# Kernel tuning notes

Hardware: AMD Instinct MI355X
Metric: run time of the kernel (lower is better)

Reference implementation:

```python
import jax, jax.numpy as jnp
import numpy as np

B, N, C = 1024, 64, 512  # batch, num_classes (graph nodes), in_channels
EPS = 1e-5  # BatchNorm1d default eps


def setup_inputs() -> dict:
    key = jax.random.key(0)
    kx, ku, kv = jax.random.split(key, 3)
    std = float(np.sqrt(2.0 / C))  # matches weight.data.normal_(0, sqrt(2/in_channels))
    return {
        "x": jax.random.normal(kx, (B, N, C), dtype=jnp.float32),
        "U_w": jax.random.normal(ku, (C, C), dtype=jnp.float32) * std,
        "U_b": jnp.zeros((C,), dtype=jnp.float32),
        "V_w": jax.random.normal(kv, (C, C), dtype=jnp.float32) * std,
        "V_b": jnp.zeros((C,), dtype=jnp.float32),
        "bn_w": jnp.ones((N,), dtype=jnp.float32),
        "bn_b": jnp.zeros((N,), dtype=jnp.float32),
        "neighbor_num": 4,
    }


def reference(x, U_w, U_b, V_w, V_b, bn_w, bn_b, neighbor_num):
    # --- dynamic top-k adjacency from dot-product similarity ('dots' metric) ---
    si = jax.lax.stop_gradient(x)                       # x.detach()
    s = jnp.einsum('bic,bjc->bij', si, si)              # [B,N,N] similarity
    thr = jax.lax.top_k(s, neighbor_num)[0][..., -1:]   # k-th largest per row
    adj = (s >= thr).astype(x.dtype)                    # [B,N,N] 0/1 adjacency
    # --- symmetric normalization D^{-1/2} A D^{-1/2} ---
    dinv = jnp.sum(adj, axis=-1) ** -0.5                # [B,N]
    A = adj * dinv[:, :, None] * dinv[:, None, :]       # diag(d) @ A @ diag(d)
    # --- aggregate: A V(x) + U(x) ---
    Vx = x @ V_w.T + V_b                                # [B,N,C]
    agg = jnp.einsum('bij,bjc->bic', A, Vx) + x @ U_w.T + U_b
    # --- BatchNorm1d over channel dim = N (training mode: batch stats over (B,C)) ---
    mean = jnp.mean(agg, axis=(0, 2), keepdims=True)
    var = jnp.mean(jnp.square(agg - mean), axis=(0, 2), keepdims=True)  # biased
    y = (agg - mean) * jax.lax.rsqrt(var + EPS) * bn_w[None, :, None] + bn_b[None, :, None]
    return jax.nn.relu(x + y)
```

## Files before the change

kernel.cpp:

```cpp
#include <hip/hip_runtime.h>
#include <stdint.h>

typedef unsigned short u16;
typedef unsigned int   u32;
typedef unsigned long long u64;

typedef __attribute__((ext_vector_type(8))) short short8;
typedef __attribute__((ext_vector_type(4))) float floatx4;
typedef __attribute__((ext_vector_type(4))) float fx4;
typedef __attribute__((ext_vector_type(2))) double dx2;

#define MFMA16(a,b,c) __builtin_amdgcn_mfma_f32_16x16x32_bf16((a),(b),(c),0,0,0)

#define GLL16(ldsptr, gptr) __builtin_amdgcn_global_load_lds( \
    (const __attribute__((address_space(1))) u32*)(gptr), \
    (__attribute__((address_space(3))) u32*)(ldsptr), 16, 0, 0)

__device__ __forceinline__ u16 f2bf(float f) {
  u32 u = __float_as_uint(f);
  return (u16)((u + 0x7FFFu + ((u >> 16) & 1u)) >> 16);
}
__device__ __forceinline__ short8 mk_frag(u64 lo, u64 hi) {
  union { short8 v; u64 q[2]; } u; u.q[0] = lo; u.q[1] = hi; return u.v;
}
__device__ __forceinline__ u64 pack4bf(float a, float b, float c, float d) {
  return (u64)f2bf(a) | ((u64)f2bf(b) << 16) | ((u64)f2bf(c) << 32) | ((u64)f2bf(d) << 48);
}

__global__ __launch_bounds__(256) void k_wcvt(const float* __restrict__ Uw,
                                              const float* __restrict__ Ub,
                                              const float* __restrict__ Vw,
                                              const float* __restrict__ Vb,
                                              u16* __restrict__ Wvu,
                                              float* __restrict__ biascat,
                                              float* __restrict__ stats) {
  int idx = blockIdx.x * 256 + threadIdx.x;
  int o  = idx >> 7;
  int k4 = (idx & 127) << 2;
  const float* src = (o < 512) ? (Vw + (size_t)o * 512 + k4)
                               : (Uw + (size_t)(o - 512) * 512 + k4);
  fx4 v = *(const fx4*)src;
  *(u64*)(Wvu + (size_t)o * 512 + k4) = pack4bf(v.x, v.y, v.z, v.w);
  if (idx < 1024) {
    biascat[idx] = (idx < 512) ? Vb[idx] : Ub[idx - 512];
    stats[idx] = 0.f;
  }
}

__global__ __launch_bounds__(256) void k_adj(const float* __restrict__ x,
                                             u16* __restrict__ xb16,
                                             u16* __restrict__ A16) {
  const int b = blockIdx.x;
  const int t = threadIdx.x;
  const int ti = t >> 4;
  const int tj = t & 15;

  __shared__ __align__(16) unsigned char smem_adj[33792 + 512 + 512];
  double* xs64     = (double*)smem_adj;
  double* s_lds    = (double*)smem_adj;
  double* thr_lds  = (double*)(smem_adj + 33792);
  double* dinv_lds = (double*)(smem_adj + 33792 + 512);

  const float* xb = x + (size_t)b * 32768;
  u16* xbg = xb16 + (size_t)b * 32768;

  double acc[4][4];
#pragma unroll
  for (int r = 0; r < 4; ++r)
#pragma unroll
    for (int c = 0; c < 4; ++c) acc[r][c] = 0.0;

  for (int k0 = 0; k0 < 512; k0 += 64) {
    __syncthreads();
#pragma unroll
    for (int i = 0; i < 4; ++i) {
      int s  = i * 256 + t;
      int row = s >> 4;
      int q4 = (s & 15) << 2;
      fx4 v = *(const fx4*)(xb + row * 512 + k0 + q4);
      dx2 d0 = {(double)v.x, (double)v.y};
      dx2 d1 = {(double)v.z, (double)v.w};
      *(dx2*)&xs64[row * 66 + q4]     = d0;
      *(dx2*)&xs64[row * 66 + q4 + 2] = d1;
      __builtin_nontemporal_store(pack4bf(v.x, v.y, v.z, v.w),
                                  (u64*)&xbg[row * 512 + k0 + q4]);
    }
    __syncthreads();
#pragma unroll 2
    for (int k = 0; k < 64; k += 4) {
      dx2 av[4][2], bv[4][2];
#pragma unroll
      for (int r = 0; r < 4; ++r) {
        av[r][0] = *(const dx2*)&xs64[(ti * 4 + r) * 66 + k];
        av[r][1] = *(const dx2*)&xs64[(ti * 4 + r) * 66 + k + 2];
      }
#pragma unroll
      for (int c = 0; c < 4; ++c) {
        bv[c][0] = *(const dx2*)&xs64[(tj + 16 * c) * 66 + k];
        bv[c][1] = *(const dx2*)&xs64[(tj + 16 * c) * 66 + k + 2];
      }
#pragma unroll
      for (int r = 0; r < 4; ++r)
#pragma unroll
        for (int c = 0; c < 4; ++c) {
          acc[r][c] += av[r][0][0] * bv[c][0][0];
          acc[r][c] += av[r][0][1] * bv[c][0][1];
          acc[r][c] += av[r][1][0] * bv[c][1][0];
          acc[r][c] += av[r][1][1] * bv[c][1][1];
        }
    }
  }
  __syncthreads();

#pragma unroll
  for (int r = 0; r < 4; ++r)
#pragma unroll
    for (int c = 0; c < 4; ++c)
      s_lds[(ti * 4 + r) * 65 + tj + 16 * c] = acc[r][c];
  __syncthreads();

  if (t < 64) {
    const double* row = &s_lds[t * 65];
    double v0 = -1e300, v1 = -1e300, v2 = -1e300, v3 = -1e300;
    for (int j = 0; j < 64; ++j) {
      double v = row[j];
      if (v > v3) {
        if (v > v2) {
          v3 = v2;
          if (v > v1) { v2 = v1; if (v > v0) { v1 = v0; v0 = v; } else { v1 = v; } }
          else { v2 = v; }
        } else { v3 = v; }
      }
    }
    int d = 0;
    for (int j = 0; j < 64; ++j) d += (row[j] >= v3) ? 1 : 0;
    thr_lds[t] = v3;
    dinv_lds[t] = 1.0 / sqrt((double)d);
  }
  __syncthreads();
  {
    int i = t >> 2;
    int j0 = (t & 3) << 4;
    double thr = thr_lds[i];
    double di = dinv_lds[i];
    const double* row = &s_lds[i * 65];
    u16* dst = A16 + (size_t)b * 4096 + i * 64 + j0;
#pragma unroll
    for (int q = 0; q < 4; ++q) {
      int j = j0 + q * 4;
      float a0 = (row[j + 0] >= thr) ? (float)(di * dinv_lds[j + 0]) : 0.f;
      float a1 = (row[j + 1] >= thr) ? (float)(di * dinv_lds[j + 1]) : 0.f;
      float a2 = (row[j + 2] >= thr) ? (float)(di * dinv_lds[j + 2]) : 0.f;
      float a3 = (row[j + 3] >= thr) ? (float)(di * dinv_lds[j + 3]) : 0.f;
      *(u64*)(dst + q * 4) = pack4bf(a0, a1, a2, a3);
    }
  }
}

__device__ __forceinline__ void stage_tiles(unsigned char* base,
                                            const u16* __restrict__ xrow,
                                            const u16* __restrict__ Wvu,
                                            int c0, int k0,
                                            int w, int lane, int swb) {
#pragma unroll
  for (int i = 0; i < 2; ++i) {
    int chunk = i * 4 + w;
    int r = chunk * 8 + (lane >> 3);
    GLL16(base + chunk * 1024,
          (const unsigned char*)(xrow + r * 512 + k0) + swb);
  }
#pragma unroll
  for (int i = 0; i < 8; ++i) {
    int chunk = i * 4 + w;
    int ol = chunk * 8 + (lane >> 3);
    int o  = (ol < 128) ? (c0 + ol) : (512 + c0 + (ol - 128));
    GLL16(base + 8192 + chunk * 1024,
          (const unsigned char*)(Wvu + (size_t)o * 512 + k0) + swb);
  }
}

__global__ __launch_bounds__(256, 2) void k_gemm(const u16* __restrict__ xb16,
                                                 const u16* __restrict__ Wvu,
                                                 const u16* __restrict__ A16,
                                                 const float* __restrict__ biascat,
                                                 float* __restrict__ stats,
                                                 float* __restrict__ aggout) {
  const int orig = blockIdx.x;
  const int nid  = (orig & 7) * 512 + (orig >> 3);
  const int c0 = (nid & 3) * 128;
  const int b  = nid >> 2;

  const int t = threadIdx.x;
  const int w = t >> 6;
  const int lane = t & 63;
  const int ln = lane & 15;
  const int g4 = (lane >> 4) << 2;
  const int sws = (ln & 7) << 3;
  const int swb = ((lane & 7) ^ (lane >> 3)) << 4;

  __shared__ __align__(16) unsigned char smem[81920];
  u16*   lds_A    = (u16*)smem;
  u16*   lds_p    = (u16*)(smem + 8192);
  float* lds_stat = (float*)(smem + 40448);
  float* lds_out  = (float*)(smem + 40960);

  floatx4 acc[4][4];
#pragma unroll
  for (int mf = 0; mf < 4; ++mf)
#pragma unroll
    for (int nf = 0; nf < 4; ++nf) acc[mf][nf] = (floatx4){0.f, 0.f, 0.f, 0.f};

  const u16* xrow = xb16 + (size_t)b * 32768;

  stage_tiles(smem, xrow, Wvu, c0, 0, w, lane, swb);
  __syncthreads();

  for (int kt = 0; kt < 8; ++kt) {
    unsigned char* cur = smem + ((kt & 1) ? 40960 : 0);
    unsigned char* nxt = smem + ((kt & 1) ? 0 : 40960);

    if (kt < 7) {
      stage_tiles(nxt, xrow, Wvu, c0, (kt + 1) * 64, w, lane, swb);
    } else {
      const unsigned char* srcA = (const unsigned char*)(A16 + (size_t)b * 4096);
#pragma unroll
      for (int i = 0; i < 2; ++i) {
        int chunk = i * 4 + w;
        GLL16(nxt + chunk * 1024,
              srcA + chunk * 1024 + (lane >> 3) * 128 + swb);
      }
    }

    const u16* lds_x = (const u16*)cur;
    const u16* lds_w = (const u16*)(cur + 8192);
#pragma unroll
    for (int kk = 0; kk < 2; ++kk) {
      int kb = kk * 32 + g4;
      int kbs = kb ^ sws;
      short8 af[4];
#pragma unroll
      for (int mf = 0; mf < 4; ++mf) {
        const u16* p = &lds_x[(mf * 16 + ln) * 64];
        af[mf] = mk_frag(*(const u64*)(p + kbs), *(const u64*)(p + (kbs ^ 16)));
      }
#pragma unroll
      for (int nf = 0; nf < 4; ++nf) {
        int ol = (nf < 2) ? (w * 32 + nf * 16 + ln)
                          : (128 + w * 32 + (nf - 2) * 16 + ln);
        const u16* p = &lds_w[ol * 64];
        short8 bf = mk_frag(*(const u64*)(p + kbs), *(const u64*)(p + (kbs ^ 16)));
#pragma unroll
        for (int mf = 0; mf < 4; ++mf)
          acc[mf][nf] = MFMA16(af[mf], bf, acc[mf][nf]);
      }
    }
    __syncthreads();
  }

#pragma unroll
  for (int nf = 0; nf < 4; ++nf) {
    int o = (nf < 2) ? (c0 + w * 32 + nf * 16 + ln)
                     : (512 + c0 + w * 32 + (nf - 2) * 16 + ln);
    float bv = biascat[o];
#pragma unroll
    for (int mf = 0; mf < 4; ++mf)
#pragma unroll
      for (int r = 0; r < 4; ++r) acc[mf][nf][r] += bv;
  }

#pragma unroll
  for (int mf = 0; mf < 4; ++mf)
#pragma unroll
    for (int nf = 0; nf < 2; ++nf) {
      int c  = w * 32 + nf * 16 + ln;
      int j0 = mf * 16 + g4;
      *(u64*)&lds_p[c * 68 + j0] =
          pack4bf(acc[mf][nf][0], acc[mf][nf][1], acc[mf][nf][2], acc[mf][nf][3]);
    }
  if (t < 128) lds_stat[t] = 0.f;
  __syncthreads();

  floatx4 acc2[4][2];
#pragma unroll
  for (int mf = 0; mf < 4; ++mf)
#pragma unroll
    for (int nf = 0; nf < 2; ++nf) acc2[mf][nf] = acc[mf][nf + 2];
#pragma unroll
  for (int kk = 0; kk < 2; ++kk) {
    int kb = kk * 32 + g4;
    int kbs = kb ^ sws;
    short8 af[4];
#pragma unroll
    for (int mf = 0; mf < 4; ++mf) {
      const u16* p = &lds_A[(mf * 16 + ln) * 64];
      af[mf] = mk_frag(*(const u64*)(p + kbs), *(const u64*)(p + (kbs ^ 16)));
    }
#pragma unroll
    for (int nf = 0; nf < 2; ++nf) {
      int c = w * 32 + nf * 16 + ln;
      const u16* p = &lds_p[c * 68 + kb];
      short8 bf = mk_frag(*(const u64*)p, *(const u64*)(p + 16));
#pragma unroll
      for (int mf = 0; mf < 4; ++mf)
        acc2[mf][nf] = MFMA16(af[mf], bf, acc2[mf][nf]);
    }
  }

#pragma unroll
  for (int mf = 0; mf < 4; ++mf) {
#pragma unroll
    for (int r = 0; r < 4; ++r) {
      int i = mf * 16 + g4 + r;
      float v0 = acc2[mf][0][r];
      float v1 = acc2[mf][1][r];
      lds_out[i * 132 + w * 32 + ln]      = v0;
      lds_out[i * 132 + w * 32 + 16 + ln] = v1;
      float s = v0 + v1, ss = v0 * v0 + v1 * v1;
#pragma unroll
      for (int m = 1; m < 16; m <<= 1) { s += __shfl_xor(s, m); ss += __shfl_xor(ss, m); }
      if (ln == 0) {
        atomicAdd(&lds_stat[i * 2 + 0], s);
        atomicAdd(&lds_stat[i * 2 + 1], ss);
      }
    }
  }
  __syncthreads();

  float* outp = aggout + (size_t)b * 32768 + c0;
#pragma unroll
  for (int i8 = 0; i8 < 8; ++i8) {
    int flat = i8 * 256 + t;
    int row = flat >> 5;
    int c4 = (flat & 31) << 2;
    fx4 v = *(const fx4*)&lds_out[row * 132 + c4];
    __builtin_nontemporal_store(v, (fx4*)(outp + (size_t)row * 512 + c4));
  }
  if (t < 64) {
    float* sg = stats + ((size_t)(b & 7) * 64 + t) * 2;
    atomicAdd(&sg[0], lds_stat[t * 2 + 0]);
    atomicAdd(&sg[1], lds_stat[t * 2 + 1]);
  }
}

__global__ void k_bnfin(const float* __restrict__ stats,
                        const float* __restrict__ bnw,
                        const float* __restrict__ bnb,
                        float* __restrict__ params) {
  int t = threadIdx.x;
  if (t >= 64) return;
  float S = 0.f, SS = 0.f;
  for (int g = 0; g < 8; ++g) {
    S  += stats[((size_t)g * 64 + t) * 2 + 0];
    SS += stats[((size_t)g * 64 + t) * 2 + 1];
  }
  const float inv = 1.f / (1024.f * 512.f);
  float mean = S * inv;
  float var = SS * inv - mean * mean;
  float istd = rsqrtf(var + 1e-5f);
  params[t]       = mean;
  params[64 + t]  = istd * bnw[t];
  params[128 + t] = bnb[t];
}

__global__ __launch_bounds__(256) void k_final(const float* __restrict__ x,
                                               const float* __restrict__ params,
                                               float* __restrict__ out) {
  __shared__ float pm[64], psc[64], psh[64];
  if (threadIdx.x < 64) {
    pm[threadIdx.x]  = params[threadIdx.x];
    psc[threadIdx.x] = params[64 + threadIdx.x];
    psh[threadIdx.x] = params[128 + threadIdx.x];
  }
  __syncthreads();
  const size_t total4 = (size_t)1024 * 64 * 512 / 4;
  for (size_t i4 = (size_t)blockIdx.x * 256 + threadIdx.x; i4 < total4;
       i4 += (size_t)gridDim.x * 256) {
    int n = (int)((i4 >> 7) & 63);
    fx4 a  = ((const fx4*)out)[i4];
    fx4 xv = ((const fx4*)x)[i4];
    float m = pm[n], sc = psc[n], sh = psh[n];
    fx4 r;
    r.x = fmaxf(xv.x + (a.x - m) * sc + sh, 0.f);
    r.y = fmaxf(xv.y + (a.y - m) * sc + sh, 0.f);
    r.z = fmaxf(xv.z + (a.z - m) * sc + sh, 0.f);
    r.w = fmaxf(xv.w + (a.w - m) * sc + sh, 0.f);
    ((fx4*)out)[i4] = r;
  }
}

extern "C" void kernel_launch(void* const* d_in, const int* in_sizes, int n_in,
                              void* d_out, int out_size, void* d_ws, size_t ws_size,
                              hipStream_t stream) {
  const float* x   = (const float*)d_in[0];
  const float* Uw  = (const float*)d_in[1];
  const float* Ub  = (const float*)d_in[2];
  const float* Vw  = (const float*)d_in[3];
  const float* Vb  = (const float*)d_in[4];
  const float* bnw = (const float*)d_in[5];
  const float* bnb = (const float*)d_in[6];

  char* ws = (char*)d_ws;
  u16*  xb16    = (u16*)ws;
  u16*  A16     = (u16*)(ws + 67108864);
  u16*  Wvu     = (u16*)(ws + 75497472);
  float* biascat = (float*)(ws + 76546048);
  float* stats   = (float*)(ws + 76550144);
  float* params  = (float*)(ws + 76554240);

  float* agg = (float*)d_out;

  k_wcvt <<<dim3(512),  dim3(256), 0, stream>>>(Uw, Ub, Vw, Vb, Wvu, biascat, stats);
  k_adj  <<<dim3(1024), dim3(256), 0, stream>>>(x, xb16, A16);
  k_gemm <<<dim3(4096), dim3(256), 0, stream>>>(xb16, Wvu, A16, biascat, stats, agg);
  k_bnfin<<<dim3(1),    dim3(64),  0, stream>>>(stats, bnw, bnb, params);
  k_final<<<dim3(2048), dim3(256), 0, stream>>>(x, params, agg);
}
```

Before: 331.5 us.

## Exploit Gram symmetry in adjacency kernel, swizzle LDS, read bf16 x in epilogue

The similarity kernel now computes only the upper-triangular 4x4 tiles of the symmetric Gram matrix with 136 of 256 threads, mirroring results into LDS, and applies an XOR swizzle to the fp64 LDS tile to reduce bank conflicts. The final residual/BN/ReLU kernel reads the bf16 copy of x instead of fp32 x, halving that stream's bytes. The bf16 residual adds rounding error to the output relative to the fp32 reference, and idle threads in the Gram loop reduce parallel utilisation.

```diff
diff --git a/kernel.cpp b/kernel.cpp
--- a/kernel.cpp
+++ b/kernel.cpp
@@ -20,6 +20,7 @@
   u32 u = __float_as_uint(f);
   return (u16)((u + 0x7FFFu + ((u >> 16) & 1u)) >> 16);
 }
+__device__ __forceinline__ float bf2f(u16 h) { return __uint_as_float(((u32)h) << 16); }
 __device__ __forceinline__ short8 mk_frag(u64 lo, u64 hi) {
   union { short8 v; u64 q[2]; } u; u.q[0] = lo; u.q[1] = hi; return u.v;
 }
@@ -52,8 +53,16 @@
                                              u16* __restrict__ A16) {
   const int b = blockIdx.x;
   const int t = threadIdx.x;
-  const int ti = t >> 4;
-  const int tj = t & 15;
+
+  int ti = 0, rem = t, done = 0;
+#pragma unroll
+  for (int r = 0; r < 16; ++r) {
+    int cnt = 16 - r;
+    if (!done) { if (rem < cnt) done = 1; else { rem -= cnt; ti = r + 1; } }
+  }
+  const int tj = ti + rem;
+  const int swa = (ti & 3) << 2;
+  const int swb = (tj & 3) << 2;
 
   __shared__ __align__(16) unsigned char smem_adj[33792 + 512 + 512];
   double* xs64     = (double*)smem_adj;
@@ -77,46 +86,59 @@
       int s  = i * 256 + t;
       int row = s >> 4;
       int q4 = (s & 15) << 2;
+      int qs = q4 ^ (((row >> 2) & 3) << 2);
       fx4 v = *(const fx4*)(xb + row * 512 + k0 + q4);
       dx2 d0 = {(double)v.x, (double)v.y};
       dx2 d1 = {(double)v.z, (double)v.w};
-      *(dx2*)&xs64[row * 66 + q4]     = d0;
-      *(dx2*)&xs64[row * 66 + q4 + 2] = d1;
+      *(dx2*)&xs64[row * 66 + qs]     = d0;
+      *(dx2*)&xs64[row * 66 + qs + 2] = d1;
       __builtin_nontemporal_store(pack4bf(v.x, v.y, v.z, v.w),
                                   (u64*)&xbg[row * 512 + k0 + q4]);
     }
     __syncthreads();
+    if (t < 136) {
 #pragma unroll 2
-    for (int k = 0; k < 64; k += 4) {
-      dx2 av[4][2], bv[4][2];
-#pragma unroll
-      for (int r = 0; r < 4; ++r) {
-        av[r][0] = *(const dx2*)&xs64[(ti * 4 + r) * 66 + k];
-        av[r][1] = *(const dx2*)&xs64[(ti * 4 + r) * 66 + k + 2];
-      }
-#pragma unroll
-      for (int c = 0; c < 4; ++c) {
-        bv[c][0] = *(const dx2*)&xs64[(tj + 16 * c) * 66 + k];
-        bv[c][1] = *(const dx2*)&xs64[(tj + 16 * c) * 66 + k + 2];
-      }
+      for (int k = 0; k < 64; k += 4) {
+        int ka = k ^ swa, kb = k ^ swb;
+        dx2 av[4][2], bv[4][2];
+#pragma unroll
+        for (int r = 0; r < 4; ++r) {
+          av[r][0] = *(const dx2*)&xs64[(ti * 4 + r) * 66 + ka];
+          av[r][1] = *(const dx2*)&xs64[(ti * 4 + r) * 66 + ka + 2];
+        }
+#pragma unroll
+        for (int c = 0; c < 4; ++c) {
+          bv[c][0] = *(const dx2*)&xs64[(tj * 4 + c) * 66 + kb];
+          bv[c][1] = *(const dx2*)&xs64[(tj * 4 + c) * 66 + kb + 2];
+        }
+#pragma unroll
+        for (int r = 0; r < 4; ++r)
+#pragma unroll
+          for (int c = 0; c < 4; ++c) {
+            acc[r][c] += av[r][0][0] * bv[c][0][0];
+            acc[r][c] += av[r][0][1] * bv[c][0][1];
+            acc[r][c] += av[r][1][0] * bv[c][1][0];
+            acc[r][c] += av[r][1][1] * bv[c][1][1];
+          }
+      }
+    }
+  }
+  __syncthreads();
+
+  if (t < 136) {
+#pragma unroll
+    for (int r = 0; r < 4; ++r)
+#pragma unroll
+      for (int c = 0; c < 4; ++c)
+        s_lds[(ti * 4 + r) * 65 + tj * 4 + c] = acc[r][c];
+    if (ti != tj) {
 #pragma unroll
       for (int r = 0; r < 4; ++r)
 #pragma unroll
-        for (int c = 0; c < 4; ++c) {
-          acc[r][c] += av[r][0][0] * bv[c][0][0];
-          acc[r][c] += av[r][0][1] * bv[c][0][1];
-          acc[r][c] += av[r][1][0] * bv[c][1][0];
-          acc[r][c] += av[r][1][1] * bv[c][1][1];
-        }
-    }
-  }
-  __syncthreads();
-
-#pragma unroll
-  for (int r = 0; r < 4; ++r)
-#pragma unroll
-    for (int c = 0; c < 4; ++c)
-      s_lds[(ti * 4 + r) * 65 + tj + 16 * c] = acc[r][c];
+        for (int c = 0; c < 4; ++c)
+          s_lds[(tj * 4 + c) * 65 + ti * 4 + r] = acc[r][c];
+    }
+  }
   __syncthreads();
 
   if (t < 64) {
@@ -362,7 +384,7 @@
   params[128 + t] = bnb[t];
 }
 
-__global__ __launch_bounds__(256) void k_final(const float* __restrict__ x,
+__global__ __launch_bounds__(256) void k_final(const u16* __restrict__ xb16,
                                                const float* __restrict__ params,
                                                float* __restrict__ out) {
   __shared__ float pm[64], psc[64], psh[64];
@@ -376,14 +398,14 @@
   for (size_t i4 = (size_t)blockIdx.x * 256 + threadIdx.x; i4 < total4;
        i4 += (size_t)gridDim.x * 256) {
     int n = (int)((i4 >> 7) & 63);
-    fx4 a  = ((const fx4*)out)[i4];
-    fx4 xv = ((const fx4*)x)[i4];
+    fx4 a = ((const fx4*)out)[i4];
+    u64 xq = *(const u64*)&xb16[i4 * 4];
     float m = pm[n], sc = psc[n], sh = psh[n];
     fx4 r;
-    r.x = fmaxf(xv.x + (a.x - m) * sc + sh, 0.f);
-    r.y = fmaxf(xv.y + (a.y - m) * sc + sh, 0.f);
-    r.z = fmaxf(xv.z + (a.z - m) * sc + sh, 0.f);
-    r.w = fmaxf(xv.w + (a.w - m) * sc + sh, 0.f);
+    r.x = fmaxf(bf2f((u16)(xq      )) + (a.x - m) * sc + sh, 0.f);
+    r.y = fmaxf(bf2f((u16)(xq >> 16)) + (a.y - m) * sc + sh, 0.f);
+    r.z = fmaxf(bf2f((u16)(xq >> 32)) + (a.z - m) * sc + sh, 0.f);
+    r.w = fmaxf(bf2f((u16)(xq >> 48)) + (a.w - m) * sc + sh, 0.f);
     ((fx4*)out)[i4] = r;
   }
 }
@@ -413,5 +435,5 @@
   k_adj  <<<dim3(1024), dim3(256), 0, stream>>>(x, xb16, A16);
   k_gemm <<<dim3(4096), dim3(256), 0, stream>>>(xb16, Wvu, A16, biascat, stats, agg);
   k_bnfin<<<dim3(1),    dim3(64),  0, stream>>>(stats, bnw, bnb, params);
-  k_final<<<dim3(2048), dim3(256), 0, stream>>>(x, params, agg);
-}
+  k_final<<<dim3(2048), dim3(256), 0, stream>>>(xb16, params, agg);
+}
```

Result: faster. 316.6 us (-4.5%).
